# Optimization experiments

Hardware: AMD Instinct MI355X
Metric: run time of the kernel (lower is better)

## Reference

```python
import jax, jax.numpy as jnp
import numpy as np

N, E = 50000, 800000
IN_DIM, HIDDEN, HEADS, EDGE_DIM, OUT_DIM = 128, 64, 4, 16, 1
NEG_SLOPE = 0.2


def gat_conv(x, src, dst, edge_attr, W, We, att_src, att_dst, att_edge, bias, heads, out_ch, concat):
    n = x.shape[0]
    h = (x @ W).reshape(n, heads, out_ch)                     # [N,H,C]
    a_src = jnp.einsum('nhc,hc->nh', h, att_src)              # [N,H]
    a_dst = jnp.einsum('nhc,hc->nh', h, att_dst)
    e = (edge_attr @ We).reshape(-1, heads, out_ch)           # [E,H,C]
    a_e = jnp.einsum('ehc,hc->eh', e, att_edge)               # [E,H]
    alpha = jax.nn.leaky_relu(a_src[src] + a_dst[dst] + a_e, NEG_SLOPE)  # [E,H]
    # per-destination-node softmax
    amax = jax.ops.segment_max(alpha, dst, num_segments=n)
    ex = jnp.exp(alpha - amax[dst])
    denom = jax.ops.segment_sum(ex, dst, num_segments=n)
    alpha = ex / (denom[dst] + 1e-16)
    msg = h[src] * alpha[..., None]                           # [E,H,C]
    out = jax.ops.segment_sum(msg, dst, num_segments=n)       # [N,H,C]
    out = out.reshape(n, heads * out_ch) if concat else out.mean(axis=1)
    return out + bias


def setup_inputs() -> dict:
    key = jax.random.key(0)
    ks = jax.random.split(key, 16)
    s = 0.1
    inp = {
        'x': jax.random.normal(ks[0], (N, IN_DIM), jnp.float32),
        'edge_index': jax.random.randint(ks[1], (2, E), 0, N, jnp.int32),
        'edge_attr': jax.random.normal(ks[2], (E, EDGE_DIM), jnp.float32),
        # layer 1: heads=4, concat=True
        'W1': jax.random.normal(ks[3], (IN_DIM, HEADS * HIDDEN), jnp.float32) * s,
        'We1': jax.random.normal(ks[4], (EDGE_DIM, HEADS * HIDDEN), jnp.float32) * s,
        'as1': jax.random.normal(ks[5], (HEADS, HIDDEN), jnp.float32) * s,
        'ad1': jax.random.normal(ks[6], (HEADS, HIDDEN), jnp.float32) * s,
        'ae1': jax.random.normal(ks[7], (HEADS, HIDDEN), jnp.float32) * s,
        'b1': jnp.zeros((HEADS * HIDDEN,), jnp.float32),
        # layer 2: heads=1, concat=False
        'W2': jax.random.normal(ks[8], (HEADS * HIDDEN, HIDDEN), jnp.float32) * s,
        'We2': jax.random.normal(ks[9], (EDGE_DIM, HIDDEN), jnp.float32) * s,
        'as2': jax.random.normal(ks[10], (1, HIDDEN), jnp.float32) * s,
        'ad2': jax.random.normal(ks[11], (1, HIDDEN), jnp.float32) * s,
        'ae2': jax.random.normal(ks[12], (1, HIDDEN), jnp.float32) * s,
        'b2': jnp.zeros((HIDDEN,), jnp.float32),
        'Wlin': jax.random.normal(ks[13], (HIDDEN, OUT_DIM), jnp.float32) * s,
        'blin': jnp.zeros((OUT_DIM,), jnp.float32),
    }
    return inp


def reference(x, edge_index, edge_attr, W1, We1, as1, ad1, ae1, b1, W2, We2, as2, ad2, ae2, b2, Wlin, blin):
    src, dst = edge_index[0], edge_index[1]
    h = jax.nn.relu(gat_conv(x, src, dst, edge_attr, W1, We1, as1, ad1, ae1, b1, HEADS, HIDDEN, True))
    h = jax.nn.relu(gat_conv(h, src, dst, edge_attr, W2, We2, as2, ad2, ae2, b2, 1, HIDDEN, False))
    return h @ Wlin + blin
```

## Files before the change

kernel.cpp:

```cpp
#include <hip/hip_runtime.h>
#include <math.h>

#define IN_DIM 128
#define HID 64
#define HEADS 4
#define EDGE_DIM 16
#define L1_OUT 256
#define NEG_SLOPE 0.2f
#define PAD 64

typedef __attribute__((ext_vector_type(8))) _Float16 half8_t;
typedef __attribute__((ext_vector_type(4))) _Float16 half4_t;
typedef __attribute__((ext_vector_type(4))) float floatx4;

__global__ __launch_bounds__(256) void prep_kernel(
    const float* __restrict__ W1, const float* __restrict__ as1, const float* __restrict__ ad1,
    const float* __restrict__ W2, const float* __restrict__ as2, const float* __restrict__ ad2,
    const float* __restrict__ We1, const float* __restrict__ ae1,
    const float* __restrict__ We2, const float* __restrict__ ae2,
    _Float16* __restrict__ W1t, _Float16* __restrict__ W2t,
    float* __restrict__ q1, float* __restrict__ q2) {
    int id = blockIdx.x * 256 + threadIdx.x;
    if (id < 272 * 128) {
        int n = id >> 7, k = id & 127;
        float v = 0.f;
        if (n < 256) v = W1[k * 256 + n];
        else if (n < 260) { int h = n - 256; float s = 0.f;
            for (int c = 0; c < 64; ++c) s += W1[k * 256 + h * 64 + c] * as1[h * 64 + c]; v = s; }
        else if (n < 264) { int h = n - 260; float s = 0.f;
            for (int c = 0; c < 64; ++c) s += W1[k * 256 + h * 64 + c] * ad1[h * 64 + c]; v = s; }
        W1t[id] = (_Float16)v;
        return;
    }
    id -= 272 * 128;
    if (id < 80 * 256) {
        int n = id >> 8, k = id & 255;
        float v = 0.f;
        if (n < 64) v = W2[k * 64 + n];
        else if (n == 64) { float s = 0.f; for (int c = 0; c < 64; ++c) s += W2[k * 64 + c] * as2[c]; v = s; }
        else if (n == 65) { float s = 0.f; for (int c = 0; c < 64; ++c) s += W2[k * 64 + c] * ad2[c]; v = s; }
        W2t[id] = (_Float16)v;
        return;
    }
    id -= 80 * 256;
    if (id < 64) {
        int k = id >> 2, h = id & 3;
        float s = 0.f;
        for (int c = 0; c < 64; ++c) s += We1[k * 256 + h * 64 + c] * ae1[h * 64 + c];
        q1[id] = s;
        return;
    }
    id -= 64;
    if (id < 16) {
        float s = 0.f;
        for (int c = 0; c < 64; ++c) s += We2[id * 64 + c] * ae2[c];
        q2[id] = s;
    }
}

__global__ __launch_bounds__(256) void scatter_edge_kernel(
    const int* __restrict__ src, const int* __restrict__ dst,
    const float* __restrict__ ea, const float* __restrict__ q1,
    const float* __restrict__ q2, int* __restrict__ deg,
    float4* __restrict__ rec, int E) {
    __shared__ float q[80];
    if (threadIdx.x < 64) q[threadIdx.x] = q1[threadIdx.x];
    else if (threadIdx.x < 80) q[threadIdx.x] = q2[threadIdx.x - 64];
    __syncthreads();
    int e = blockIdx.x * 256 + threadIdx.x;
    if (e >= E) return;
    const float4* p = (const float4*)(ea + (size_t)e * EDGE_DIM);
    float4 v0 = p[0], v1 = p[1], v2 = p[2], v3 = p[3];
    int sn = src[e];
    int d = dst[e];
    float a[16] = {v0.x, v0.y, v0.z, v0.w, v1.x, v1.y, v1.z, v1.w,
                   v2.x, v2.y, v2.z, v2.w, v3.x, v3.y, v3.z, v3.w};
    float4 r1;
    float* rp = (float*)&r1;
#pragma unroll
    for (int h = 0; h < 4; ++h) {
        float s = 0.f;
#pragma unroll
        for (int k = 0; k < 16; ++k) s += a[k] * q[k * 4 + h];
        rp[h] = s;
    }
    float r2 = 0.f;
#pragma unroll
    for (int k = 0; k < 16; ++k) r2 += a[k] * q[64 + k];
    int rank = atomicAdd(&deg[d], 1);
    if (rank >= PAD) return;
    size_t pos = (size_t)d * PAD + rank;
    float4 lo;
    lo.x = __int_as_float(sn); lo.y = r2; lo.z = 0.f; lo.w = 0.f;
    rec[pos * 2] = lo;
    rec[pos * 2 + 1] = r1;
}

template <int NTOT, int NFEAT, int HATT, int KD, bool A32>
__global__ __launch_bounds__(256) void gemm_att_kernel(
    const void* __restrict__ Av, const _Float16* __restrict__ Bt,
    _Float16* __restrict__ C, float* __restrict__ asrc, float* __restrict__ adst,
    int M) {
    constexpr int KC = KD / 32;
    const int tid = threadIdx.x;
    const int lane = tid & 63;
    const int w = tid >> 6;
    const int m = lane & 15;
    const int quad = lane >> 4;
    const int row0 = blockIdx.x * 64;
    const int arow = row0 + w * 16 + m;
    const bool rv = arow < M;

    half8_t af[KC];
    if constexpr (A32) {
        const float* A = (const float*)Av + (size_t)arow * KD + quad * 8;
#pragma unroll
        for (int kc = 0; kc < KC; ++kc) {
            float4 f0 = {}, f1 = {};
            if (rv) {
                f0 = *(const float4*)(A + kc * 32);
                f1 = *(const float4*)(A + kc * 32 + 4);
            }
            af[kc] = (half8_t){(_Float16)f0.x, (_Float16)f0.y, (_Float16)f0.z, (_Float16)f0.w,
                               (_Float16)f1.x, (_Float16)f1.y, (_Float16)f1.z, (_Float16)f1.w};
        }
    } else {
        const _Float16* A = (const _Float16*)Av + (size_t)arow * KD + quad * 8;
#pragma unroll
        for (int kc = 0; kc < KC; ++kc) {
            half8_t a = {};
            if (rv) a = *(const half8_t*)(A + kc * 32);
            af[kc] = a;
        }
    }

    floatx4 acc[NTOT];
#pragma unroll
    for (int t = 0; t < NTOT; ++t) acc[t] = (floatx4){0.f, 0.f, 0.f, 0.f};
    const _Float16* Bp = Bt + (size_t)m * KD + quad * 8;
#pragma unroll
    for (int kc = 0; kc < KC; ++kc) {
#pragma unroll
        for (int t = 0; t < NTOT; ++t) {
            half8_t bf = *(const half8_t*)(Bp + (size_t)t * 16 * KD + kc * 32);
            acc[t] = __builtin_amdgcn_mfma_f32_16x16x32_f16(af[kc], bf, acc[t], 0, 0, 0);
        }
    }

    const int TE = NFEAT / 16;
#pragma unroll
    for (int r = 0; r < 4; ++r) {
        int orow = row0 + w * 16 + quad * 4 + r;
        if (orow >= M) continue;
#pragma unroll
        for (int t = 0; t < TE; ++t)
            C[(size_t)orow * NFEAT + t * 16 + m] = (_Float16)acc[t][r];
        float v = acc[TE][r];
        if (m < HATT) asrc[orow * HATT + m] = v;
        else if (m < 2 * HATT) adst[orow * HATT + (m - HATT)] = v;
    }
}

__global__ __launch_bounds__(256) void node1_kernel(
    const int* __restrict__ deg, const float4* __restrict__ rec,
    const float* __restrict__ asrc1, const float* __restrict__ adst1,
    const _Float16* __restrict__ h1, const float* __restrict__ b1,
    _Float16* __restrict__ hr1, int Nn) {
    int lane = threadIdx.x & 63, wv = threadIdx.x >> 6;
    int n = blockIdx.x * 4 + wv;
    if (n >= Nn) return;
    int dg = __builtin_amdgcn_readfirstlane(deg[n]);
    if (dg > PAD) dg = PAD;
    const int j16 = lane & 15;
    const int hh = lane >> 4;
    const int ebase = lane & 48;
    float adn = adst1[n * 4 + hh];
    const int* reci = (const int*)rec;
    const float* recf = (const float*)rec;
    size_t s0 = (size_t)n * PAD;

    float ax = 0.f, ay = 0.f, az = 0.f, aw = 0.f, lsum = 0.f;
    for (int c0 = 0; c0 < dg; c0 += 16) {
        int rem = dg - c0; if (rem > 16) rem = 16;
        size_t srec = s0 + c0 + (j16 < rem ? j16 : 0);
        int si = reci[srec * 8];
        float qv = recf[srec * 8 + 4 + hh];
        float av = asrc1[si * 4 + hh];
        half4_t v[16];
#pragma unroll
        for (int j = 0; j < 16; ++j) {
            int idx = __shfl(si, j);
            v[j] = *(const half4_t*)(h1 + (size_t)idx * L1_OUT + lane * 4);
        }
        float t = qv + av + adn;
        float e = (j16 < rem) ? __expf(t > 0.f ? t : NEG_SLOPE * t) : 0.f;
        lsum += e;
#pragma unroll
        for (int j = 0; j < 16; ++j) {
            float ej = __shfl(e, ebase | j);
            ax += ej * (float)v[j].x;
            ay += ej * (float)v[j].y;
            az += ej * (float)v[j].z;
            aw += ej * (float)v[j].w;
        }
    }
#pragma unroll
    for (int o = 1; o < 16; o <<= 1) lsum += __shfl_xor(lsum, o);
    float inv = 1.f / (lsum + 1e-16f);
    float4 bb = *(const float4*)(b1 + lane * 4);
    half4_t out;
    out.x = (_Float16)fmaxf(ax * inv + bb.x, 0.f);
    out.y = (_Float16)fmaxf(ay * inv + bb.y, 0.f);
    out.z = (_Float16)fmaxf(az * inv + bb.z, 0.f);
    out.w = (_Float16)fmaxf(aw * inv + bb.w, 0.f);
    *(half4_t*)(hr1 + (size_t)n * L1_OUT + lane * 4) = out;
}

__global__ __launch_bounds__(256) void node2_kernel(
    const int* __restrict__ deg, const float4* __restrict__ rec,
    const float* __restrict__ asrc2, const float* __restrict__ adst2,
    const _Float16* __restrict__ h2, const float* __restrict__ b2,
    const float* __restrict__ Wlin, const float* __restrict__ blin,
    float* __restrict__ out, int Nn) {
    int lane = threadIdx.x & 63, wv = threadIdx.x >> 6;
    int n = blockIdx.x * 4 + wv;
    if (n >= Nn) return;
    int dg = __builtin_amdgcn_readfirstlane(deg[n]);
    if (dg > PAD) dg = PAD;
    const int j16 = lane & 15;
    size_t s0 = (size_t)n * PAD;
    float adn = adst2[n];
    const int* reci = (const int*)rec;
    const float* recf = (const float*)rec;

    float lsum = 0.f, acc = 0.f;
    for (int c0 = 0; c0 < dg; c0 += 16) {
        int rem = dg - c0; if (rem > 16) rem = 16;
        size_t srec = s0 + c0 + (j16 < rem ? j16 : 0);
        int si = reci[srec * 8];
        float qv = recf[srec * 8 + 1];
        float av = asrc2[si];
        _Float16 v[16];
#pragma unroll
        for (int j = 0; j < 16; ++j) {
            int idx = __shfl(si, j);
            v[j] = h2[(size_t)idx * HID + lane];
        }
        float t = qv + av + adn;
        float e = (j16 < rem) ? __expf(t > 0.f ? t : NEG_SLOPE * t) : 0.f;
        lsum += e;
#pragma unroll
        for (int j = 0; j < 16; ++j) {
            float ej = __shfl(e, j);
            acc += ej * (float)v[j];
        }
    }
#pragma unroll
    for (int o = 1; o < 16; o <<= 1) lsum += __shfl_xor(lsum, o);
    float res = fmaxf(acc / (lsum + 1e-16f) + b2[lane], 0.f);
    float t2 = res * Wlin[lane];
    for (int o = 32; o > 0; o >>= 1) t2 += __shfl_down(t2, o);
    if (lane == 0) out[n] = t2 + blin[0];
}

extern "C" void kernel_launch(void* const* d_in, const int* in_sizes, int n_in,
                              void* d_out, int out_size, void* d_ws, size_t ws_size,
                              hipStream_t stream) {
    const float* x    = (const float*)d_in[0];
    const int*   ei   = (const int*)d_in[1];
    const float* ea   = (const float*)d_in[2];
    const float* W1   = (const float*)d_in[3];
    const float* We1  = (const float*)d_in[4];
    const float* as1  = (const float*)d_in[5];
    const float* ad1  = (const float*)d_in[6];
    const float* ae1  = (const float*)d_in[7];
    const float* b1   = (const float*)d_in[8];
    const float* W2   = (const float*)d_in[9];
    const float* We2  = (const float*)d_in[10];
    const float* as2  = (const float*)d_in[11];
    const float* ad2  = (const float*)d_in[12];
    const float* ae2  = (const float*)d_in[13];
    const float* b2   = (const float*)d_in[14];
    const float* Wlin = (const float*)d_in[15];
    const float* blin = (const float*)d_in[16];

    const int N = in_sizes[0] / IN_DIM;
    const int E = in_sizes[1] / 2;
    const int* src = ei;
    const int* dst = ei + E;

    char* base = (char*)d_ws;
    size_t off = 0;
    auto alloc = [&](size_t bytes) -> char* {
        char* p = base + off;
        off = (off + bytes + 255) & ~(size_t)255;
        return p;
    };
    int*      deg     = (int*)alloc((size_t)N * 4);
    float*    q1      = (float*)alloc(64 * 4);
    float*    q2      = (float*)alloc(16 * 4);
    _Float16* W1t     = (_Float16*)alloc((size_t)272 * 128 * 2);
    _Float16* W2t     = (_Float16*)alloc((size_t)80 * 256 * 2);
    float4*   rec     = (float4*)alloc((size_t)N * PAD * 32);
    float*    asrc1   = (float*)alloc((size_t)N * 4 * 4);
    float*    adst1   = (float*)alloc((size_t)N * 4 * 4);
    _Float16* h1      = (_Float16*)alloc((size_t)N * L1_OUT * 2);
    _Float16* hr1     = (_Float16*)alloc((size_t)N * L1_OUT * 2);
    _Float16* h2      = (_Float16*)alloc((size_t)N * HID * 2);
    float*    asrc2   = (float*)alloc((size_t)N * 4);
    float*    adst2   = (float*)alloc((size_t)N * 4);
    (void)ws_size; (void)n_in; (void)out_size;

    hipMemsetAsync(deg, 0, (size_t)N * 4, stream);
    prep_kernel<<<218, 256, 0, stream>>>(W1, as1, ad1, W2, as2, ad2,
                                         We1, ae1, We2, ae2, W1t, W2t, q1, q2);
    scatter_edge_kernel<<<(E + 255) / 256, 256, 0, stream>>>(src, dst, ea, q1, q2, deg,
                                                             rec, E);

    int mbl = (N + 63) / 64;
    gemm_att_kernel<17, 256, 4, 128, true><<<mbl, 256, 0, stream>>>(x, W1t, h1, asrc1,
                                                                    adst1, N);
    node1_kernel<<<(N + 3) / 4, 256, 0, stream>>>(deg, rec, asrc1, adst1, h1, b1, hr1, N);
    gemm_att_kernel<5, 64, 1, 256, false><<<mbl, 256, 0, stream>>>(hr1, W2t, h2, asrc2,
                                                                   adst2, N);
    node2_kernel<<<(N + 3) / 4, 256, 0, stream>>>(deg, rec, asrc2, adst2, h2, b2,
                                                  Wlin, blin, (float*)d_out, N);
}
```

Measured before the change: 346.7 us.

## Split layer-1 node aggregation across two waves and prefetch next edge chunk

Layer-1 aggregation now assigns two wavefronts per destination node, each covering half of the 256 features (two heads) with half2 gathers, which doubles the wave count and reduces per-lane registers. It also prefetches the next 16-edge chunk's record indices and attention terms while the current chunk's gathers are in flight. The cost is duplicated edge-record reads and exp work per node, along with narrower 4-byte gather loads. The softmax denominator is now taken from the head's own 16-lane group via shuffle, not from the reduced lsum on each lane.

```diff
diff --git a/kernel.cpp b/kernel.cpp
--- a/kernel.cpp
+++ b/kernel.cpp
@@ -11,6 +11,7 @@
 
 typedef __attribute__((ext_vector_type(8))) _Float16 half8_t;
 typedef __attribute__((ext_vector_type(4))) _Float16 half4_t;
+typedef __attribute__((ext_vector_type(2))) _Float16 half2_t;
 typedef __attribute__((ext_vector_type(4))) float floatx4;
 
 __global__ __launch_bounds__(256) void prep_kernel(
@@ -167,53 +168,68 @@
     const _Float16* __restrict__ h1, const float* __restrict__ b1,
     _Float16* __restrict__ hr1, int Nn) {
     int lane = threadIdx.x & 63, wv = threadIdx.x >> 6;
-    int n = blockIdx.x * 4 + wv;
+    int n = blockIdx.x * 2 + (wv >> 1);
+    int half = wv & 1;
     if (n >= Nn) return;
     int dg = __builtin_amdgcn_readfirstlane(deg[n]);
     if (dg > PAD) dg = PAD;
     const int j16 = lane & 15;
     const int hh = lane >> 4;
-    const int ebase = lane & 48;
+    const int nh = half * 2 + (lane >> 5);
+    const int ebase = nh << 4;
     float adn = adst1[n * 4 + hh];
     const int* reci = (const int*)rec;
     const float* recf = (const float*)rec;
     size_t s0 = (size_t)n * PAD;
-
-    float ax = 0.f, ay = 0.f, az = 0.f, aw = 0.f, lsum = 0.f;
+    const _Float16* hbase = h1 + half * 128 + lane * 2;
+
+    float ax = 0.f, ay = 0.f, lsum = 0.f;
+    int si = 0; float qv = 0.f, av = 0.f;
+    if (dg > 0) {
+        int rem0 = dg < 16 ? dg : 16;
+        size_t sr = s0 + (j16 < rem0 ? j16 : 0);
+        si = reci[sr * 8];
+        qv = recf[sr * 8 + 4 + hh];
+        av = asrc1[si * 4 + hh];
+    }
     for (int c0 = 0; c0 < dg; c0 += 16) {
-        int rem = dg - c0; if (rem > 16) rem = 16;
-        size_t srec = s0 + c0 + (j16 < rem ? j16 : 0);
-        int si = reci[srec * 8];
-        float qv = recf[srec * 8 + 4 + hh];
-        float av = asrc1[si * 4 + hh];
-        half4_t v[16];
+        int remc = dg - c0; if (remc > 16) remc = 16;
+        half2_t v[16];
 #pragma unroll
         for (int j = 0; j < 16; ++j) {
             int idx = __shfl(si, j);
-            v[j] = *(const half4_t*)(h1 + (size_t)idx * L1_OUT + lane * 4);
+            v[j] = *(const half2_t*)(hbase + (size_t)idx * L1_OUT);
+        }
+        int si_n = 0; float qv_n = 0.f, av_n = 0.f;
+        int c1 = c0 + 16;
+        if (c1 < dg) {
+            int rem_n = dg - c1; if (rem_n > 16) rem_n = 16;
+            size_t sr = s0 + c1 + (j16 < rem_n ? j16 : 0);
+            si_n = reci[sr * 8];
+            qv_n = recf[sr * 8 + 4 + hh];
+            av_n = asrc1[si_n * 4 + hh];
         }
         float t = qv + av + adn;
-        float e = (j16 < rem) ? __expf(t > 0.f ? t : NEG_SLOPE * t) : 0.f;
+        float e = (j16 < remc) ? __expf(t > 0.f ? t : NEG_SLOPE * t) : 0.f;
         lsum += e;
 #pragma unroll
         for (int j = 0; j < 16; ++j) {
             float ej = __shfl(e, ebase | j);
             ax += ej * (float)v[j].x;
             ay += ej * (float)v[j].y;
-            az += ej * (float)v[j].z;
-            aw += ej * (float)v[j].w;
-        }
+        }
+        si = si_n; qv = qv_n; av = av_n;
     }
 #pragma unroll
     for (int o = 1; o < 16; o <<= 1) lsum += __shfl_xor(lsum, o);
-    float inv = 1.f / (lsum + 1e-16f);
-    float4 bb = *(const float4*)(b1 + lane * 4);
-    half4_t out;
-    out.x = (_Float16)fmaxf(ax * inv + bb.x, 0.f);
-    out.y = (_Float16)fmaxf(ay * inv + bb.y, 0.f);
-    out.z = (_Float16)fmaxf(az * inv + bb.z, 0.f);
-    out.w = (_Float16)fmaxf(aw * inv + bb.w, 0.f);
-    *(half4_t*)(hr1 + (size_t)n * L1_OUT + lane * 4) = out;
+    float denom = __shfl(lsum, ebase);
+    float inv = 1.f / (denom + 1e-16f);
+    const float* bp = b1 + half * 128 + lane * 2;
+    float b0 = bp[0], bb1 = bp[1];
+    half2_t out;
+    out.x = (_Float16)fmaxf(ax * inv + b0, 0.f);
+    out.y = (_Float16)fmaxf(ay * inv + bb1, 0.f);
+    *(half2_t*)(hr1 + (size_t)n * L1_OUT + half * 128 + lane * 2) = out;
 }
 
 __global__ __launch_bounds__(256) void node2_kernel(
@@ -320,7 +336,7 @@
     int mbl = (N + 63) / 64;
     gemm_att_kernel<17, 256, 4, 128, true><<<mbl, 256, 0, stream>>>(x, W1t, h1, asrc1,
                                                                     adst1, N);
-    node1_kernel<<<(N + 3) / 4, 256, 0, stream>>>(deg, rec, asrc1, adst1, h1, b1, hr1, N);
+    node1_kernel<<<(N + 1) / 2, 256, 0, stream>>>(deg, rec, asrc1, adst1, h1, b1, hr1, N);
     gemm_att_kernel<5, 64, 1, 256, false><<<mbl, 256, 0, stream>>>(hr1, W2t, h2, asrc2,
                                                                    adst2, N);
     node2_kernel<<<(N + 3) / 4, 256, 0, stream>>>(deg, rec, asrc2, adst2, h2, b2,
```

Measured after the change: 357.1 us. 1.03x slower.
